# Kernel tuning notes

Measured on AMD Instinct MI355X. Metric: run time of the kernel, lower is better.

## Reference

```python
import jax, jax.numpy as jnp
import numpy as np

B, N, A = 2, 4096, 5
TOPK = 30
K_RBF = 16
MAX_AA = 22
MAXREL = 32
EDGE_IN = 16 + K_RBF * 25 + 14 + 16  # 446
EDGE_FEAT = 128
PI = 3.1415926


def l2norm(v, eps=1e-12):
    n = jnp.sqrt(jnp.sum(v * v, axis=-1, keepdims=True))
    return v / jnp.maximum(n, eps)


def gather_nodes(nodes, idx):
    # nodes: (B,N,C), idx: (B,N,K) -> (B,N,K,C)
    b, n, k = idx.shape
    flat = idx.reshape(b, n * k, 1)
    out = jnp.take_along_axis(nodes, flat, axis=1)
    return out.reshape(b, n, k, nodes.shape[-1])


def quaternions(R):
    # R: (...,3,3) -> unit quaternion (...,4)
    Rxx, Ryy, Rzz = R[..., 0, 0], R[..., 1, 1], R[..., 2, 2]
    mag = 0.5 * jnp.sqrt(jnp.abs(1.0 + jnp.stack([Rxx - Ryy - Rzz, -Rxx + Ryy - Rzz, -Rxx - Ryy + Rzz], -1)) + 1e-12)
    signs = jnp.sign(jnp.stack([R[..., 2, 1] - R[..., 1, 2], R[..., 0, 2] - R[..., 2, 0], R[..., 1, 0] - R[..., 0, 1]], -1))
    xyz = signs * mag
    w = jnp.sqrt(jax.nn.relu(1.0 + Rxx + Ryy + Rzz) + 1e-12)[..., None] / 2.0
    return l2norm(jnp.concatenate([xyz, w], -1))


def setup_inputs():
    key = jax.random.key(0)
    ks = jax.random.split(key, 12)
    X = jax.random.normal(ks[0], (B, N, A, 3), jnp.float32) * 3.0
    mask = jnp.ones((B, N), jnp.float32)
    mask_atoms = jnp.ones((B, N, A), jnp.float32)
    means = jax.random.normal(ks[1], (K_RBF,), jnp.float32)
    stds = jax.random.normal(ks[2], (K_RBF,), jnp.float32)
    mul_w = jax.random.normal(ks[3], (A * A,), jnp.float32)
    bias_w = jax.random.normal(ks[4], (A * A,), jnp.float32)
    aa_pair_embed = jax.random.normal(ks[5], (MAX_AA * MAX_AA, K_RBF), jnp.float32) * 0.02
    aa_pair_embed = aa_pair_embed.at[441].set(0.0)  # padding_idx
    relpos_embed = jax.random.normal(ks[6], (2 * MAXREL + 1, 16), jnp.float32) * 0.02
    mask_embed = jax.random.normal(ks[7], (2, 16), jnp.float32) * 0.02
    W1 = jax.random.normal(ks[8], (EDGE_IN, EDGE_IN), jnp.float32) / np.sqrt(EDGE_IN)
    b1 = jnp.zeros((EDGE_IN,), jnp.float32)
    W2 = jax.random.normal(ks[9], (EDGE_IN, EDGE_FEAT), jnp.float32) / np.sqrt(EDGE_IN)
    b2 = jnp.zeros((EDGE_FEAT,), jnp.float32)
    aa = jax.random.randint(ks[10], (B, N), 0, 21, jnp.int32)
    residue_idx = jnp.tile(jnp.arange(N, dtype=jnp.int32)[None, :], (B, 1))
    chain_labels = jax.random.randint(ks[11], (B, N), 0, 2, jnp.int32)
    return dict(X=X, mask=mask, mask_atoms=mask_atoms, means=means, stds=stds, mul_w=mul_w,
                bias_w=bias_w, aa_pair_embed=aa_pair_embed, relpos_embed=relpos_embed,
                mask_embed=mask_embed, W1=W1, b1=b1, W2=W2, b2=b2, aa=aa,
                residue_idx=residue_idx, chain_labels=chain_labels)


def reference(X, mask, mask_atoms, means, stds, mul_w, bias_w, aa_pair_embed, relpos_embed,
              mask_embed, W1, b1, W2, b2, aa, residue_idx, chain_labels):
    Ca = X[:, :, 1]  # (B,N,3) C-alpha
    # ---- _dist: spatial kNN over C-alpha ----
    mask2d = mask[:, :, None] * mask[:, None, :]
    dx = Ca[:, None, :, :] - Ca[:, :, None, :]
    D = mask2d * jnp.sqrt(jnp.sum(dx * dx, -1) + 1e-6)
    D_adj = D + (1.0 - mask2d) * jnp.max(D, -1, keepdims=True)
    _, E_idx = jax.lax.top_k(-D_adj, TOPK)  # smallest distances
    mask_attend = jnp.take_along_axis(mask2d, E_idx, axis=2)  # (B,N,K)
    # ---- orientation features (local frames + quaternions) ----
    ones3 = jnp.ones((B, 1, 3), X.dtype)
    u = l2norm(jnp.concatenate([ones3, Ca[:, 1:] - Ca[:, :-1]], 1))
    b_ = l2norm(jnp.concatenate([u[:, :-1] - u[:, 1:], ones3], 1))
    n_ = l2norm(jnp.concatenate([jnp.cross(u[:, :-1], u[:, 1:]), ones3], 1))
    lf = jnp.stack([b_, n_, jnp.cross(b_, n_)], axis=2)  # (B,N,3,3)
    X_nb = gather_nodes(Ca, E_idx)                       # (B,N,K,3)
    O_nb = gather_nodes(lf.reshape(B, N, 9), E_idx).reshape(B, N, TOPK, 3, 3)
    t = X_nb - Ca[:, :, None, :]
    t = jnp.einsum('bnij,bnkj->bnki', lf, t)
    t = l2norm(t) * mask_attend[..., None]
    r = jnp.einsum('bnji,bnkjl->bnkil', lf, O_nb)  # lf^T @ O_nb
    q = quaternions(r) * mask_attend[..., None]
    O_feat = jnp.concatenate([t, q, 1.0 - 2.0 * jnp.abs(t), 1.0 - 2.0 * jnp.abs(q)], -1)  # (B,N,K,14)
    # ---- positional / chain embeddings ----
    offset = residue_idx[:, :, None] - residue_idx[:, None, :]
    offset_nb = jnp.take_along_axis(offset, E_idx, 2)
    d_chain = (chain_labels[:, :, None] == chain_labels[:, None, :]).astype(jnp.int32)
    E_chains = jnp.take_along_axis(d_chain, E_idx, 2)
    d = jnp.clip(offset_nb + MAXREL, 0, 2 * MAXREL)
    E_pos = relpos_embed[d] + mask_embed[E_chains]  # (B,N,K,16)
    # ---- GaussianLayer: aa-pair embed + atom-pair distance RBF ----
    aa_pair = aa[:, :, None] * MAX_AA + aa[:, None, :]
    aa_nb = jnp.take_along_axis(aa_pair, E_idx, 2)
    feat_aapair = aa_pair_embed[aa_nb] * mask_attend[..., None]  # (B,N,K,16)
    nbX = gather_nodes(X.reshape(B, N, A * 3), E_idx).reshape(B, N, TOPK, A, 3)
    delta = nbX[:, :, :, :, None, :] - X[:, :, None, None, :, :]  # (B,N,K,A,A,3)
    Dab = jnp.sqrt(jnp.sum(delta * delta, -1) + 1e-12)            # (B,N,K,A,A)
    et = jnp.arange(A * A).reshape(A, A)
    xg = mul_w[et] * Dab + bias_w[et]
    m_nb = gather_nodes(mask_atoms, E_idx)  # (B,N,K,A)
    xg = xg * (m_nb[..., None, :] * m_nb[..., :, None])
    std = jnp.abs(stds) + 0.01
    g = jnp.exp(-0.5 * ((xg[..., None] - means) / std) ** 2) / ((2.0 * PI) ** 0.5 * std)
    gbf = g.reshape(B, N, TOPK, A * A * K_RBF) * mask_attend[..., None]  # (B,N,K,400)
    # ---- fuse and project (NonLinear gbf_proj) ----
    E = jnp.concatenate([E_pos, gbf, O_feat, feat_aapair], -1)  # (B,N,K,446)
    h = jax.nn.gelu(E @ W1 + b1, approximate=False)
    return h @ W2 + b2  # (B,N,K,128)
```

## Files before the change

kernel.cpp:

```cpp
#include <hip/hip_runtime.h>
#include <cstdint>
#include <cstddef>

#define NN 4096
#define TOPK_ 30
#define BN_TOT 8192
#define M_TOT 245760
#define KP 448
#define HSTRIDE 136
#define EF 128

typedef unsigned short u16;
typedef unsigned int u32;
typedef __attribute__((ext_vector_type(8))) short bf16x8;
typedef __attribute__((ext_vector_type(4))) float f32x4;

__device__ __forceinline__ float b2f(u16 u){ return __uint_as_float(((u32)u)<<16); }
__device__ __forceinline__ u16 f2b(float f){
  u32 u = __float_as_uint(f);
  return (u16)((u + 0x7FFFu + ((u>>16)&1u)) >> 16);
}
__device__ __forceinline__ float ldf(const void* p, long i, int fl){
  return fl ? ((const float*)p)[i] : b2f(((const u16*)p)[i]);
}
__device__ __forceinline__ int is_f32_flag(const u16* mask){
  return (((const u32*)mask)[0] == 0x3F800000u) ? 1 : 0;
}
__device__ __forceinline__ void norm3(float x,float y,float z,float&ox,float&oy,float&oz){
  float n = sqrtf(x*x+y*y+z*z); n = fmaxf(n, 1e-12f);
  ox=x/n; oy=y/n; oz=z/n;
}
__device__ __forceinline__ float sgn(float x){ return x>0.f?1.f:(x<0.f?-1.f:0.f); }
__device__ __forceinline__ float gelu_fast(float x){
  float y = 0.70710678118654752440f * x;
  float s = fabsf(y);
  float t = __builtin_amdgcn_rcpf(fmaf(0.3275911f, s, 1.0f));
  float p = fmaf(fmaf(fmaf(fmaf(1.061405429f, t, -1.453152027f), t, 1.421413741f), t,
                 -0.284496736f), t, 0.254829592f);
  float e = __expf(-y*y);
  float erfs = fmaf(-p*t, e, 1.0f);
  float erfy = (x >= 0.f) ? erfs : -erfs;
  float hx = 0.5f*x;
  return fmaf(hx, erfy, hx);
}
__device__ __forceinline__ u32 pk_bf16(float lo, float hi){
  u32 r;
  asm("v_cvt_pk_bf16_f32 %0, %1, %2" : "=v"(r) : "v"(lo), "v"(hi));
  return r;
}

__global__ __launch_bounds__(256) void prep_kernel(
    const void* __restrict__ X, const u16* __restrict__ mask,
    const void* __restrict__ W1, const void* __restrict__ b1,
    const void* __restrict__ W2, const void* __restrict__ b2,
    float* __restrict__ ca, float* __restrict__ lf,
    u16* __restrict__ W1P, u16* __restrict__ W2P,
    float* __restrict__ b1p, float* __restrict__ b2p)
{
  const int fl = is_f32_flag(mask);
  int idx = blockIdx.x*256 + threadIdx.x;
  if (idx < BN_TOT) {
    int i = idx & (NN-1);
    float cax = ldf(X, (long)idx*15+3, fl), cay = ldf(X, (long)idx*15+4, fl), caz = ldf(X, (long)idx*15+5, fl);
    ca[idx*4+0]=cax; ca[idx*4+1]=cay; ca[idx*4+2]=caz; ca[idx*4+3]=0.f;
    float bx,by,bz,nx,ny,nz;
    if (i < NN-1) {
      float uix,uiy,uiz;
      if (i==0) { norm3(1.f,1.f,1.f,uix,uiy,uiz); }
      else {
        float px=ldf(X,(long)(idx-1)*15+3,fl), py=ldf(X,(long)(idx-1)*15+4,fl), pz=ldf(X,(long)(idx-1)*15+5,fl);
        norm3(cax-px, cay-py, caz-pz, uix,uiy,uiz);
      }
      float qx=ldf(X,(long)(idx+1)*15+3,fl), qy=ldf(X,(long)(idx+1)*15+4,fl), qz=ldf(X,(long)(idx+1)*15+5,fl);
      float vx,vy,vz; norm3(qx-cax, qy-cay, qz-caz, vx,vy,vz);
      norm3(uix-vx, uiy-vy, uiz-vz, bx,by,bz);
      norm3(uiy*vz-uiz*vy, uiz*vx-uix*vz, uix*vy-uiy*vx, nx,ny,nz);
    } else {
      norm3(1.f,1.f,1.f,bx,by,bz); nx=bx; ny=by; nz=bz;
    }
    float cx = by*nz - bz*ny, cy = bz*nx - bx*nz, cz = bx*ny - by*nx;
    float* L = lf + (size_t)idx*12;
    L[0]=bx;L[1]=by;L[2]=bz;L[3]=nx;L[4]=ny;L[5]=nz;L[6]=cx;L[7]=cy;L[8]=cz;
    return;
  }
  int r1 = idx - BN_TOT;
  if (r1 < 229376) {
    int f = r1 >> 9, li = r1 & 511;
    int n0 = f / 14, kc = f - n0*14;
    int ln = li >> 3, j = li & 7;
    int n = n0*16 + (ln & 15);
    int k = kc*32 + (ln >> 4)*8 + j;
    W1P[r1] = (n < 446 && k < 446) ? (fl ? f2b(((const float*)W1)[(long)k*446 + n])
                                         : ((const u16*)W1)[(long)k*446 + n]) : (u16)0;
    return;
  }
  int r2 = r1 - 229376;
  if (r2 < 65536) {
    int f = r2 >> 9, li = r2 & 511;
    int n0 = f >> 4, kc = f & 15;
    int ln = li >> 3, j = li & 7;
    int n = n0*16 + (ln & 15);
    int k = kc*32 + (ln >> 4)*8 + j;
    W2P[r2] = (k < 446) ? (fl ? f2b(((const float*)W2)[(long)k*128 + n])
                              : ((const u16*)W2)[(long)k*128 + n]) : (u16)0;
    return;
  }
  int r3 = r2 - 65536;
  if (r3 < 512) { b1p[r3] = (r3<446)? ldf(b1, r3, fl) : 0.f; return; }
  int r4 = r3 - 512;
  if (r4 < 128) { b2p[r4] = ldf(b2, r4, fl); }
}

__global__ __launch_bounds__(64) void knn_kernel(const float4* __restrict__ ca,
                                                 int* __restrict__ eidx)
{
#pragma clang fp contract(off)
  __shared__ u32 keys[NN];
  int bi = blockIdx.x;
  int lane = threadIdx.x;
  int b = bi >> 12;
  const float4 ci = ca[bi];
  const float4* cab = ca + (b<<12);
  u32 mind = 0xFFFFFFFFu; int minj = 1<<30; int minslot = 0;
  for (int c = 0; c < 64; ++c) {
    int j = (c<<6) | lane;
    float4 cj = cab[j];
    float dx = cj.x-ci.x, dy = cj.y-ci.y, dz = cj.z-ci.z;
    float ss = dx*dx;
    ss = ss + dy*dy;
    ss = ss + dz*dz;
    float d = sqrtf(ss + 1e-6f);
    u32 db = __float_as_uint(d);
    keys[(c<<6)|lane] = db;
    if (db < mind) { mind = db; minj = j; minslot = c; }
  }
  __syncthreads();
  for (int r = 0; r < TOPK_; ++r) {
    u32 wd = mind; int wj = minj;
    #pragma unroll
    for (int off = 32; off; off >>= 1) {
      u32 od = __shfl_xor(wd, off, 64);
      int oj = __shfl_xor(wj, off, 64);
      if (od < wd || (od == wd && oj < wj)) { wd = od; wj = oj; }
    }
    if (lane == 0) eidx[bi*TOPK_ + r] = wj;
    if ((wj & 63) == lane && wj == minj) {
      keys[minslot*64 + lane] = 0xFFFFFFFFu;
      mind = 0xFFFFFFFFu; minj = 1<<30;
      for (int c = 0; c < 64; ++c) {
        u32 db = keys[(c<<6)|lane];
        if (db < mind) { mind = db; minj = (c<<6)|lane; minslot = c; }
      }
    }
  }
}

__global__ __launch_bounds__(512,2) void mega_mlp(
    const void* __restrict__ X, const u16* __restrict__ mask, const void* __restrict__ mask_atoms,
    const void* __restrict__ means, const void* __restrict__ stds,
    const void* __restrict__ mul_w, const void* __restrict__ bias_w,
    const void* __restrict__ aa_pe, const void* __restrict__ relpos, const void* __restrict__ mask_emb,
    const int* __restrict__ aa, const int* __restrict__ ridx, const int* __restrict__ chains,
    const int* __restrict__ eidx, const float* __restrict__ ca, const float* __restrict__ lf,
    const u16* __restrict__ W1P, const u16* __restrict__ W2P,
    const float* __restrict__ b1p, const float* __restrict__ b2p,
    void* __restrict__ C)
{
  __shared__ __align__(16) u16 Et[128*448];
  __shared__ float Dabs[128][29];
  __shared__ float maA[128];
  const int fl = is_f32_flag(mask);
  int tid = threadIdx.x;
  int lane = tid & 63, wave = tid >> 6;
  int wr = wave >> 2, wc = wave & 3;
  int rowBase = blockIdx.x * 128;

  {
    int eo = tid >> 2, q = tid & 3;
    int e = rowBase + eo;
    int bi = (int)((unsigned)e / 30u);
    int k = e - bi*30;
    int bj = ((bi >> 12) << 12) + eidx[bi*TOPK_ + k];
    if (q == 1) maA[eo] = ldf(mask, bi, fl) * ldf(mask, bj, fl);
    float Xi[15];
    #pragma unroll
    for (int v = 0; v < 15; ++v) Xi[v] = ldf(X, (long)bi*15 + v, fl);
    for (int a = q; a < 5; a += 4) {
      float xj0 = ldf(X,(long)bj*15 + a*3+0, fl);
      float xj1 = ldf(X,(long)bj*15 + a*3+1, fl);
      float xj2 = ldf(X,(long)bj*15 + a*3+2, fl);
      float mja = ldf(mask_atoms,(long)bj*5 + a, fl);
      #pragma unroll
      for (int c = 0; c < 5; ++c) {
        float d0 = xj0 - Xi[c*3+0];
        float d1 = xj1 - Xi[c*3+1];
        float d2 = xj2 - Xi[c*3+2];
        float Dab = sqrtf(d0*d0 + d1*d1 + d2*d2 + 1e-12f);
        float mm = mja * ldf(mask_atoms,(long)bj*5 + c, fl);
        float mw = ldf(mul_w, a*5+c, fl), bw = ldf(bias_w, a*5+c, fl);
        Dabs[eo][a*5+c] = (mw*Dab + bw) * mm;
      }
    }
  }

  if (tid < 128) {
    int eo = tid;
    int e = rowBase + eo;
    int bi = (int)((unsigned)e / 30u);
    int k = e - bi*30;
    int bj = ((bi >> 12) << 12) + eidx[bi*TOPK_ + k];
    float ma = ldf(mask, bi, fl) * ldf(mask, bj, fl);
    char* rowB = (char*)Et + eo*896;
    int xr = (eo & 7) << 4;
    int d = ridx[bi] - ridx[bj] + 32; d = d < 0 ? 0 : (d > 64 ? 64 : d);
    int ch = (chains[bi] == chains[bj]) ? 1 : 0;
    float rp[16];
    #pragma unroll
    for (int f = 0; f < 16; ++f)
      rp[f] = ldf(relpos, d*16 + f, fl) + ldf(mask_emb, ch*16 + f, fl);
    {
      uint4 wA, wB;
      wA.x = pk_bf16(rp[0],rp[1]);  wA.y = pk_bf16(rp[2],rp[3]);
      wA.z = pk_bf16(rp[4],rp[5]);  wA.w = pk_bf16(rp[6],rp[7]);
      wB.x = pk_bf16(rp[8],rp[9]);  wB.y = pk_bf16(rp[10],rp[11]);
      wB.z = pk_bf16(rp[12],rp[13]);wB.w = pk_bf16(rp[14],rp[15]);
      *(uint4*)(rowB + (0 ^ xr))  = wA;
      *(uint4*)(rowB + (16 ^ xr)) = wB;
    }
    float Li[9], Lj[9];
    #pragma unroll
    for (int q_ = 0; q_ < 9; ++q_) { Li[q_] = lf[(size_t)bi*12+q_]; Lj[q_] = lf[(size_t)bj*12+q_]; }
    float dx = ca[bj*4+0]-ca[bi*4+0], dy = ca[bj*4+1]-ca[bi*4+1], dz = ca[bj*4+2]-ca[bi*4+2];
    float t0 = Li[0]*dx+Li[1]*dy+Li[2]*dz;
    float t1 = Li[3]*dx+Li[4]*dy+Li[5]*dz;
    float t2 = Li[6]*dx+Li[7]*dy+Li[8]*dz;
    float tn = fmaxf(sqrtf(t0*t0+t1*t1+t2*t2), 1e-12f);
    t0 = t0/tn*ma; t1 = t1/tn*ma; t2 = t2/tn*ma;
    float R00=Li[0]*Lj[0]+Li[3]*Lj[3]+Li[6]*Lj[6];
    float R01=Li[0]*Lj[1]+Li[3]*Lj[4]+Li[6]*Lj[7];
    float R02=Li[0]*Lj[2]+Li[3]*Lj[5]+Li[6]*Lj[8];
    float R10=Li[1]*Lj[0]+Li[4]*Lj[3]+Li[7]*Lj[6];
    float R11=Li[1]*Lj[1]+Li[4]*Lj[4]+Li[7]*Lj[7];
    float R12=Li[1]*Lj[2]+Li[4]*Lj[5]+Li[7]*Lj[8];
    float R20=Li[2]*Lj[0]+Li[5]*Lj[3]+Li[8]*Lj[6];
    float R21=Li[2]*Lj[1]+Li[5]*Lj[4]+Li[8]*Lj[7];
    float R22=Li[2]*Lj[2]+Li[5]*Lj[5]+Li[8]*Lj[8];
    float m0 = 0.5f*sqrtf(fabsf(1.f+R00-R11-R22)+1e-12f);
    float m1 = 0.5f*sqrtf(fabsf(1.f-R00+R11-R22)+1e-12f);
    float m2 = 0.5f*sqrtf(fabsf(1.f-R00-R11+R22)+1e-12f);
    float q0 = sgn(R21-R12)*m0, q1 = sgn(R02-R20)*m1, q2 = sgn(R10-R01)*m2;
    float qw = 0.5f*sqrtf(fmaxf(1.f+R00+R11+R22, 0.f)+1e-12f);
    float qn = fmaxf(sqrtf(q0*q0+q1*q1+q2*q2+qw*qw), 1e-12f);
    q0 = q0/qn*ma; q1 = q1/qn*ma; q2 = q2/qn*ma; qw = qw/qn*ma;
    int aap = aa[bi]*22 + aa[bj];
    float av[16];
    #pragma unroll
    for (int f = 0; f < 16; ++f) av[f] = ldf(aa_pe, aap*16 + f, fl) * ma;
    uint4 w0, w1, w2, w3;
    w0.x = pk_bf16(t0, t1);                     w0.y = pk_bf16(t2, q0);
    w0.z = pk_bf16(q1, q2);                     w0.w = pk_bf16(qw, 1.f-2.f*fabsf(t0));
    w1.x = pk_bf16(1.f-2.f*fabsf(t1), 1.f-2.f*fabsf(t2));
    w1.y = pk_bf16(1.f-2.f*fabsf(q0), 1.f-2.f*fabsf(q1));
    w1.z = pk_bf16(1.f-2.f*fabsf(q2), 1.f-2.f*fabsf(qw));
    w1.w = pk_bf16(av[0], av[1]);
    w2.x = pk_bf16(av[2], av[3]);   w2.y = pk_bf16(av[4], av[5]);
    w2.z = pk_bf16(av[6], av[7]);   w2.w = pk_bf16(av[8], av[9]);
    w3.x = pk_bf16(av[10], av[11]); w3.y = pk_bf16(av[12], av[13]);
    w3.z = pk_bf16(av[14], av[15]); w3.w = 0u;
    *(uint4*)(rowB + (832 ^ xr)) = w0;
    *(uint4*)(rowB + (848 ^ xr)) = w1;
    *(uint4*)(rowB + (864 ^ xr)) = w2;
    *(uint4*)(rowB + (880 ^ xr)) = w3;
  }
  __syncthreads();

  {
    float meanv[16], rinvv[16], coefv[16];
    #pragma unroll
    for (int r = 0; r < 16; ++r) {
      meanv[r] = ldf(means, r, fl);
      float sd = fabsf(ldf(stds, r, fl)) + 0.01f;
      rinvv[r] = 1.0f / sd;
      coefv[r] = 0.3989422804014327f * rinvv[r];
    }
    #pragma unroll 1
    for (int i = 0; i < 13; ++i) {
      int G = tid + i*512;
      if (G < 6400) {
        int row = (int)((unsigned)G / 50u);
        int gp = G - row*50;
        float xg = Dabs[row][gp >> 1];
        float ma = maA[row];
        int odd = gp & 1;
        u32 w[4];
        #pragma unroll
        for (int j2 = 0; j2 < 4; ++j2) {
          float me0 = odd ? meanv[j2*2+8]   : meanv[j2*2];
          float ri0 = odd ? rinvv[j2*2+8]   : rinvv[j2*2];
          float co0 = odd ? coefv[j2*2+8]   : coefv[j2*2];
          float me1 = odd ? meanv[j2*2+9]   : meanv[j2*2+1];
          float ri1 = odd ? rinvv[j2*2+9]   : rinvv[j2*2+1];
          float co1 = odd ? coefv[j2*2+9]   : coefv[j2*2+1];
          float z0 = (xg - me0) * ri0;
          float z1 = (xg - me1) * ri1;
          float v0 = __expf(-0.5f*z0*z0) * co0 * ma;
          float v1 = __expf(-0.5f*z1*z1) * co1 * ma;
          w[j2] = pk_bf16(v0, v1);
        }
        uint4 W4; W4.x = w[0]; W4.y = w[1]; W4.z = w[2]; W4.w = w[3];
        *(uint4*)((char*)Et + row*896 + ((32 + (gp<<4)) ^ ((row&7)<<4))) = W4;
      }
    }
  }
  __syncthreads();

  f32x4 acc1[4][4][2] = {};
  #pragma unroll 1
  for (int t = 0; t < 7; ++t) {
    bf16x8 af[2][4];
    #pragma unroll
    for (int kk = 0; kk < 2; ++kk)
      #pragma unroll
      for (int r = 0; r < 4; ++r) {
        int row = wr*64 + r*16 + (lane&15);
        int s = kk*4 + (lane>>4);
        af[kk][r] = *(const bf16x8*)(Et + row*448 + t*64 + ((s ^ (row&7))<<3));
      }
    bf16x8 bgA[2][2][2];
    #pragma unroll
    for (int c = 0; c < 2; ++c)
      #pragma unroll
      for (int cc = 0; cc < 2; ++cc)
        #pragma unroll
        for (int kk = 0; kk < 2; ++kk)
          bgA[c][cc][kk] = *(const bf16x8*)(W1P + (((c*8 + wc*2 + cc)*14 + t*2 + kk) << 9) + lane*8);
    #pragma unroll
    for (int c = 0; c < 2; ++c)
      #pragma unroll
      for (int r = 0; r < 4; ++r)
        #pragma unroll
        for (int cc = 0; cc < 2; ++cc)
          #pragma unroll
          for (int kk = 0; kk < 2; ++kk)
            acc1[c][r][cc] = __builtin_amdgcn_mfma_f32_16x16x32_bf16(af[kk][r], bgA[c][cc][kk], acc1[c][r][cc], 0,0,0);
    bf16x8 bgB[2][2][2];
    #pragma unroll
    for (int c = 0; c < 2; ++c)
      #pragma unroll
      for (int cc = 0; cc < 2; ++cc)
        #pragma unroll
        for (int kk = 0; kk < 2; ++kk)
          bgB[c][cc][kk] = *(const bf16x8*)(W1P + ((((c+2)*8 + wc*2 + cc)*14 + t*2 + kk) << 9) + lane*8);
    #pragma unroll
    for (int c = 0; c < 2; ++c)
      #pragma unroll
      for (int r = 0; r < 4; ++r)
        #pragma unroll
        for (int cc = 0; cc < 2; ++cc)
          #pragma unroll
          for (int kk = 0; kk < 2; ++kk)
            acc1[c+2][r][cc] = __builtin_amdgcn_mfma_f32_16x16x32_bf16(af[kk][r], bgB[c][cc][kk], acc1[c+2][r][cc], 0,0,0);
  }

  u16* hs0 = Et;
  u16* hs1 = Et + 128*HSTRIDE;
  #define STORE_HS(cN, buf) do {                                                  \
    _Pragma("unroll")                                                             \
    for (int r = 0; r < 4; ++r) {                                                 \
      _Pragma("unroll")                                                           \
      for (int cc = 0; cc < 2; ++cc) {                                            \
        int col = wc*32 + cc*16 + (lane & 15);                                    \
        float bv = b1p[(cN)*128 + col];                                           \
        int row0 = wr*64 + r*16 + (lane>>4)*4;                                    \
        u32 p01 = pk_bf16(gelu_fast(acc1[cN][r][cc][0]+bv),                       \
                          gelu_fast(acc1[cN][r][cc][1]+bv));                      \
        u32 p23 = pk_bf16(gelu_fast(acc1[cN][r][cc][2]+bv),                       \
                          gelu_fast(acc1[cN][r][cc][3]+bv));                      \
        u16* hb_ = (buf) + row0*HSTRIDE + col;                                    \
        hb_[0]         = (u16)p01; hb_[HSTRIDE]   = (u16)(p01>>16);               \
        hb_[2*HSTRIDE] = (u16)p23; hb_[3*HSTRIDE] = (u16)(p23>>16);               \
      }                                                                           \
    }                                                                             \
  } while(0)

  f32x4 acc2[4][2] = {};
  __syncthreads();
  STORE_HS(0, hs0);
  __syncthreads();
  #pragma unroll
  for (int c = 0; c < 4; ++c) {
    u16* hb = (c & 1) ? hs1 : hs0;
    u16* hn = (c & 1) ? hs0 : hs1;
    if (c < 3) STORE_HS(c+1, hn);
    #pragma unroll
    for (int k2 = 0; k2 < 4; ++k2) {
      bf16x8 af2[4], bg2[2];
      #pragma unroll
      for (int r = 0; r < 4; ++r) {
        int row = wr*64 + r*16 + (lane&15);
        af2[r] = *(const bf16x8*)(hb + row*HSTRIDE + k2*32 + (lane>>4)*8);
      }
      #pragma unroll
      for (int cc = 0; cc < 2; ++cc)
        bg2[cc] = *(const bf16x8*)(W2P + ((((wc*2+cc)*16) + c*4 + k2) << 9) + lane*8);
      #pragma unroll
      for (int r = 0; r < 4; ++r)
        #pragma unroll
        for (int cc = 0; cc < 2; ++cc)
          acc2[r][cc] = __builtin_amdgcn_mfma_f32_16x16x32_bf16(af2[r], bg2[cc], acc2[r][cc], 0,0,0);
    }
    __syncthreads();
  }
  #undef STORE_HS

  const int f32out = is_f32_flag(mask);
  #pragma unroll
  for (int r = 0; r < 4; ++r) {
    #pragma unroll
    for (int cc = 0; cc < 2; ++cc) {
      int col = wc*32 + cc*16 + (lane & 15);
      float bv = b2p[col];
      #pragma unroll
      for (int g = 0; g < 4; ++g) {
        long row = (long)rowBase + wr*64 + r*16 + (lane>>4)*4 + g;
        float v = acc2[r][cc][g] + bv;
        long o = row*EF + col;
        if (f32out) ((float*)C)[o] = v;
        else        ((u16*)C)[o]  = f2b(v);
      }
    }
  }
}

extern "C" void kernel_launch(void* const* d_in, const int* in_sizes, int n_in,
                              void* d_out, int out_size, void* d_ws, size_t ws_size,
                              hipStream_t stream) {
  const void* X          = d_in[0];
  const u16* mask        = (const u16*)d_in[1];
  const void* mask_atoms = d_in[2];
  const void* means      = d_in[3];
  const void* stds       = d_in[4];
  const void* mul_w      = d_in[5];
  const void* bias_w     = d_in[6];
  const void* aa_pe      = d_in[7];
  const void* relpos     = d_in[8];
  const void* mask_emb   = d_in[9];
  const void* W1         = d_in[10];
  const void* b1         = d_in[11];
  const void* W2         = d_in[12];
  const void* b2         = d_in[13];
  const int* aa          = (const int*)d_in[14];
  const int* ridx        = (const int*)d_in[15];
  const int* chains      = (const int*)d_in[16];

  char* ws = (char*)d_ws;
  float* ca  = (float*)(ws + 0);
  float* lf  = (float*)(ws + 131072);
  int* eidx  = (int*)(ws + 524288);
  u16* W1P   = (u16*)(ws + 1507328);
  u16* W2P   = (u16*)(ws + 1966080);
  float* b1p = (float*)(ws + 2097152);
  float* b2p = (float*)(ws + 2099200);

  prep_kernel<<<1187, 256, 0, stream>>>(X, mask, W1, b1, W2, b2, ca, lf, W1P, W2P, b1p, b2p);
  knn_kernel<<<BN_TOT, 64, 0, stream>>>((const float4*)ca, eidx);
  mega_mlp<<<M_TOT/128, 512, 0, stream>>>(X, mask, mask_atoms, means, stds, mul_w, bias_w,
                                          aa_pe, relpos, mask_emb, aa, ridx, chains,
                                          eidx, ca, lf, W1P, W2P, b1p, b2p, d_out);
}
```

Measured before the change: 773.3 us.

## Use column-wise min tracking in kNN top-k and narrow edge-feature register scopes

The kNN top-k selection stops having a single lane rescan all 64 of its keys after each extraction. Each lane now keeps the minimum of one column, so only the winning column is updated: each lane reads one key of that column and a wave shuffle reduction picks its new minimum. This replaces a serial 64-step scan with a parallel reduction, at the cost of a barrier per round. Separately, the edge feature builder in the MLP kernel is restructured into scoped blocks that pack and store each uint4 immediately, which is meant to shorten register live ranges in a 512-thread kernel.

```diff
diff --git a/kernel.cpp b/kernel.cpp
--- a/kernel.cpp
+++ b/kernel.cpp
@@ -121,7 +121,7 @@
   int b = bi >> 12;
   const float4 ci = ca[bi];
   const float4* cab = ca + (b<<12);
-  u32 mind = 0xFFFFFFFFu; int minj = 1<<30; int minslot = 0;
+  u32 mind = 0xFFFFFFFFu; int minj = 1<<30;
   for (int c = 0; c < 64; ++c) {
     int j = (c<<6) | lane;
     float4 cj = cab[j];
@@ -132,7 +132,7 @@
     float d = sqrtf(ss + 1e-6f);
     u32 db = __float_as_uint(d);
     keys[(c<<6)|lane] = db;
-    if (db < mind) { mind = db; minj = j; minslot = c; }
+    if (db < mind) { mind = db; minj = j; }
   }
   __syncthreads();
   for (int r = 0; r < TOPK_; ++r) {
@@ -144,14 +144,18 @@
       if (od < wd || (od == wd && oj < wj)) { wd = od; wj = oj; }
     }
     if (lane == 0) eidx[bi*TOPK_ + r] = wj;
-    if ((wj & 63) == lane && wj == minj) {
-      keys[minslot*64 + lane] = 0xFFFFFFFFu;
-      mind = 0xFFFFFFFFu; minj = 1<<30;
-      for (int c = 0; c < 64; ++c) {
-        u32 db = keys[(c<<6)|lane];
-        if (db < mind) { mind = db; minj = (c<<6)|lane; minslot = c; }
-      }
-    }
+    int wl = wj & 63;
+    if (lane == wl) keys[wj] = 0xFFFFFFFFu;
+    __syncthreads();
+    u32 kv = keys[(lane<<6)|wl];
+    int kj = (lane<<6)|wl;
+    #pragma unroll
+    for (int off = 32; off; off >>= 1) {
+      u32 od = __shfl_xor(kv, off, 64);
+      int oj = __shfl_xor(kj, off, 64);
+      if (od < kv || (od == kv && oj < kj)) { kv = od; kj = oj; }
+    }
+    if (lane == wl) { mind = kv; minj = kj; }
   }
 }
 
@@ -212,65 +216,89 @@
     float ma = ldf(mask, bi, fl) * ldf(mask, bj, fl);
     char* rowB = (char*)Et + eo*896;
     int xr = (eo & 7) << 4;
-    int d = ridx[bi] - ridx[bj] + 32; d = d < 0 ? 0 : (d > 64 ? 64 : d);
-    int ch = (chains[bi] == chains[bj]) ? 1 : 0;
-    float rp[16];
-    #pragma unroll
-    for (int f = 0; f < 16; ++f)
-      rp[f] = ldf(relpos, d*16 + f, fl) + ldf(mask_emb, ch*16 + f, fl);
-    {
-      uint4 wA, wB;
-      wA.x = pk_bf16(rp[0],rp[1]);  wA.y = pk_bf16(rp[2],rp[3]);
-      wA.z = pk_bf16(rp[4],rp[5]);  wA.w = pk_bf16(rp[6],rp[7]);
-      wB.x = pk_bf16(rp[8],rp[9]);  wB.y = pk_bf16(rp[10],rp[11]);
-      wB.z = pk_bf16(rp[12],rp[13]);wB.w = pk_bf16(rp[14],rp[15]);
-      *(uint4*)(rowB + (0 ^ xr))  = wA;
+    {
+      int d = ridx[bi] - ridx[bj] + 32; d = d < 0 ? 0 : (d > 64 ? 64 : d);
+      int ch = (chains[bi] == chains[bj]) ? 1 : 0;
+      uint4 wA;
+      wA.x = pk_bf16(ldf(relpos,d*16+0,fl)+ldf(mask_emb,ch*16+0,fl),
+                     ldf(relpos,d*16+1,fl)+ldf(mask_emb,ch*16+1,fl));
+      wA.y = pk_bf16(ldf(relpos,d*16+2,fl)+ldf(mask_emb,ch*16+2,fl),
+                     ldf(relpos,d*16+3,fl)+ldf(mask_emb,ch*16+3,fl));
+      wA.z = pk_bf16(ldf(relpos,d*16+4,fl)+ldf(mask_emb,ch*16+4,fl),
+                     ldf(relpos,d*16+5,fl)+ldf(mask_emb,ch*16+5,fl));
+      wA.w = pk_bf16(ldf(relpos,d*16+6,fl)+ldf(mask_emb,ch*16+6,fl),
+                     ldf(relpos,d*16+7,fl)+ldf(mask_emb,ch*16+7,fl));
+      *(uint4*)(rowB + (0 ^ xr)) = wA;
+      uint4 wB;
+      wB.x = pk_bf16(ldf(relpos,d*16+8,fl)+ldf(mask_emb,ch*16+8,fl),
+                     ldf(relpos,d*16+9,fl)+ldf(mask_emb,ch*16+9,fl));
+      wB.y = pk_bf16(ldf(relpos,d*16+10,fl)+ldf(mask_emb,ch*16+10,fl),
+                     ldf(relpos,d*16+11,fl)+ldf(mask_emb,ch*16+11,fl));
+      wB.z = pk_bf16(ldf(relpos,d*16+12,fl)+ldf(mask_emb,ch*16+12,fl),
+                     ldf(relpos,d*16+13,fl)+ldf(mask_emb,ch*16+13,fl));
+      wB.w = pk_bf16(ldf(relpos,d*16+14,fl)+ldf(mask_emb,ch*16+14,fl),
+                     ldf(relpos,d*16+15,fl)+ldf(mask_emb,ch*16+15,fl));
       *(uint4*)(rowB + (16 ^ xr)) = wB;
     }
-    float Li[9], Lj[9];
-    #pragma unroll
-    for (int q_ = 0; q_ < 9; ++q_) { Li[q_] = lf[(size_t)bi*12+q_]; Lj[q_] = lf[(size_t)bj*12+q_]; }
-    float dx = ca[bj*4+0]-ca[bi*4+0], dy = ca[bj*4+1]-ca[bi*4+1], dz = ca[bj*4+2]-ca[bi*4+2];
-    float t0 = Li[0]*dx+Li[1]*dy+Li[2]*dz;
-    float t1 = Li[3]*dx+Li[4]*dy+Li[5]*dz;
-    float t2 = Li[6]*dx+Li[7]*dy+Li[8]*dz;
-    float tn = fmaxf(sqrtf(t0*t0+t1*t1+t2*t2), 1e-12f);
-    t0 = t0/tn*ma; t1 = t1/tn*ma; t2 = t2/tn*ma;
-    float R00=Li[0]*Lj[0]+Li[3]*Lj[3]+Li[6]*Lj[6];
-    float R01=Li[0]*Lj[1]+Li[3]*Lj[4]+Li[6]*Lj[7];
-    float R02=Li[0]*Lj[2]+Li[3]*Lj[5]+Li[6]*Lj[8];
-    float R10=Li[1]*Lj[0]+Li[4]*Lj[3]+Li[7]*Lj[6];
-    float R11=Li[1]*Lj[1]+Li[4]*Lj[4]+Li[7]*Lj[7];
-    float R12=Li[1]*Lj[2]+Li[4]*Lj[5]+Li[7]*Lj[8];
-    float R20=Li[2]*Lj[0]+Li[5]*Lj[3]+Li[8]*Lj[6];
-    float R21=Li[2]*Lj[1]+Li[5]*Lj[4]+Li[8]*Lj[7];
-    float R22=Li[2]*Lj[2]+Li[5]*Lj[5]+Li[8]*Lj[8];
-    float m0 = 0.5f*sqrtf(fabsf(1.f+R00-R11-R22)+1e-12f);
-    float m1 = 0.5f*sqrtf(fabsf(1.f-R00+R11-R22)+1e-12f);
-    float m2 = 0.5f*sqrtf(fabsf(1.f-R00-R11+R22)+1e-12f);
-    float q0 = sgn(R21-R12)*m0, q1 = sgn(R02-R20)*m1, q2 = sgn(R10-R01)*m2;
-    float qw = 0.5f*sqrtf(fmaxf(1.f+R00+R11+R22, 0.f)+1e-12f);
-    float qn = fmaxf(sqrtf(q0*q0+q1*q1+q2*q2+qw*qw), 1e-12f);
-    q0 = q0/qn*ma; q1 = q1/qn*ma; q2 = q2/qn*ma; qw = qw/qn*ma;
+    float t0,t1,t2,q0,q1,q2,qw;
+    {
+      float Li[9], Lj[9];
+      #pragma unroll
+      for (int q_ = 0; q_ < 9; ++q_) { Li[q_] = lf[(size_t)bi*12+q_]; Lj[q_] = lf[(size_t)bj*12+q_]; }
+      float dx = ca[bj*4+0]-ca[bi*4+0], dy = ca[bj*4+1]-ca[bi*4+1], dz = ca[bj*4+2]-ca[bi*4+2];
+      t0 = Li[0]*dx+Li[1]*dy+Li[2]*dz;
+      t1 = Li[3]*dx+Li[4]*dy+Li[5]*dz;
+      t2 = Li[6]*dx+Li[7]*dy+Li[8]*dz;
+      float tn = fmaxf(sqrtf(t0*t0+t1*t1+t2*t2), 1e-12f);
+      t0 = t0/tn*ma; t1 = t1/tn*ma; t2 = t2/tn*ma;
+      float R00=Li[0]*Lj[0]+Li[3]*Lj[3]+Li[6]*Lj[6];
+      float R01=Li[0]*Lj[1]+Li[3]*Lj[4]+Li[6]*Lj[7];
+      float R02=Li[0]*Lj[2]+Li[3]*Lj[5]+Li[6]*Lj[8];
+      float R10=Li[1]*Lj[0]+Li[4]*Lj[3]+Li[7]*Lj[6];
+      float R11=Li[1]*Lj[1]+Li[4]*Lj[4]+Li[7]*Lj[7];
+      float R12=Li[1]*Lj[2]+Li[4]*Lj[5]+Li[7]*Lj[8];
+      float R20=Li[2]*Lj[0]+Li[5]*Lj[3]+Li[8]*Lj[6];
+      float R21=Li[2]*Lj[1]+Li[5]*Lj[4]+Li[8]*Lj[7];
+      float R22=Li[2]*Lj[2]+Li[5]*Lj[5]+Li[8]*Lj[8];
+      float m0 = 0.5f*sqrtf(fabsf(1.f+R00-R11-R22)+1e-12f);
+      float m1 = 0.5f*sqrtf(fabsf(1.f-R00+R11-R22)+1e-12f);
+      float m2 = 0.5f*sqrtf(fabsf(1.f-R00-R11+R22)+1e-12f);
+      q0 = sgn(R21-R12)*m0; q1 = sgn(R02-R20)*m1; q2 = sgn(R10-R01)*m2;
+      qw = 0.5f*sqrtf(fmaxf(1.f+R00+R11+R22, 0.f)+1e-12f);
+      float qn = fmaxf(sqrtf(q0*q0+q1*q1+q2*q2+qw*qw), 1e-12f);
+      q0 = q0/qn*ma; q1 = q1/qn*ma; q2 = q2/qn*ma; qw = qw/qn*ma;
+    }
     int aap = aa[bi]*22 + aa[bj];
-    float av[16];
-    #pragma unroll
-    for (int f = 0; f < 16; ++f) av[f] = ldf(aa_pe, aap*16 + f, fl) * ma;
-    uint4 w0, w1, w2, w3;
-    w0.x = pk_bf16(t0, t1);                     w0.y = pk_bf16(t2, q0);
-    w0.z = pk_bf16(q1, q2);                     w0.w = pk_bf16(qw, 1.f-2.f*fabsf(t0));
-    w1.x = pk_bf16(1.f-2.f*fabsf(t1), 1.f-2.f*fabsf(t2));
-    w1.y = pk_bf16(1.f-2.f*fabsf(q0), 1.f-2.f*fabsf(q1));
-    w1.z = pk_bf16(1.f-2.f*fabsf(q2), 1.f-2.f*fabsf(qw));
-    w1.w = pk_bf16(av[0], av[1]);
-    w2.x = pk_bf16(av[2], av[3]);   w2.y = pk_bf16(av[4], av[5]);
-    w2.z = pk_bf16(av[6], av[7]);   w2.w = pk_bf16(av[8], av[9]);
-    w3.x = pk_bf16(av[10], av[11]); w3.y = pk_bf16(av[12], av[13]);
-    w3.z = pk_bf16(av[14], av[15]); w3.w = 0u;
-    *(uint4*)(rowB + (832 ^ xr)) = w0;
-    *(uint4*)(rowB + (848 ^ xr)) = w1;
-    *(uint4*)(rowB + (864 ^ xr)) = w2;
-    *(uint4*)(rowB + (880 ^ xr)) = w3;
+    {
+      uint4 w0;
+      w0.x = pk_bf16(t0, t1);  w0.y = pk_bf16(t2, q0);
+      w0.z = pk_bf16(q1, q2);  w0.w = pk_bf16(qw, 1.f-2.f*fabsf(t0));
+      *(uint4*)(rowB + (832 ^ xr)) = w0;
+    }
+    {
+      uint4 w1;
+      w1.x = pk_bf16(1.f-2.f*fabsf(t1), 1.f-2.f*fabsf(t2));
+      w1.y = pk_bf16(1.f-2.f*fabsf(q0), 1.f-2.f*fabsf(q1));
+      w1.z = pk_bf16(1.f-2.f*fabsf(q2), 1.f-2.f*fabsf(qw));
+      w1.w = pk_bf16(ldf(aa_pe, aap*16+0, fl)*ma, ldf(aa_pe, aap*16+1, fl)*ma);
+      *(uint4*)(rowB + (848 ^ xr)) = w1;
+    }
+    {
+      uint4 w2;
+      w2.x = pk_bf16(ldf(aa_pe, aap*16+2, fl)*ma, ldf(aa_pe, aap*16+3, fl)*ma);
+      w2.y = pk_bf16(ldf(aa_pe, aap*16+4, fl)*ma, ldf(aa_pe, aap*16+5, fl)*ma);
+      w2.z = pk_bf16(ldf(aa_pe, aap*16+6, fl)*ma, ldf(aa_pe, aap*16+7, fl)*ma);
+      w2.w = pk_bf16(ldf(aa_pe, aap*16+8, fl)*ma, ldf(aa_pe, aap*16+9, fl)*ma);
+      *(uint4*)(rowB + (864 ^ xr)) = w2;
+    }
+    {
+      uint4 w3;
+      w3.x = pk_bf16(ldf(aa_pe, aap*16+10, fl)*ma, ldf(aa_pe, aap*16+11, fl)*ma);
+      w3.y = pk_bf16(ldf(aa_pe, aap*16+12, fl)*ma, ldf(aa_pe, aap*16+13, fl)*ma);
+      w3.z = pk_bf16(ldf(aa_pe, aap*16+14, fl)*ma, ldf(aa_pe, aap*16+15, fl)*ma);
+      w3.w = 0u;
+      *(uint4*)(rowB + (880 ^ xr)) = w3;
+    }
   }
   __syncthreads();
 
```

New measurement: 728.8 us. 1.06x faster.
